# Performance work log

Measured on AMD Instinct MI355X. Metric: run time of the kernel, lower is better.

The kernel has to match this reference:

```python
import jax, jax.numpy as jnp
import numpy as np

B, T, C, HD = 16, 2048, 1024, 64


def setup_inputs() -> dict:
    key = jax.random.key(0)
    kx, kk, kq, kv = jax.random.split(key, 4)
    x = jax.random.normal(kx, (B, T, C), dtype=jnp.float32)
    Wk = jax.random.normal(kk, (C, HD), dtype=jnp.float32) * (C ** -0.5)
    Wq = jax.random.normal(kq, (C, HD), dtype=jnp.float32) * (C ** -0.5)
    Wv = jax.random.normal(kv, (C, HD), dtype=jnp.float32) * (C ** -0.5)
    return {"x": x, "Wk": Wk, "Wq": Wq, "Wv": Wv}


def reference(x, Wk, Wq, Wv):
    Bs, Ts, Cs = x.shape
    k = x @ Wk  # [B,T,HD]
    q = x @ Wq
    v = x @ Wv
    # Faithful to original: scores = key @ query^T, scaled by 1/sqrt(C) (embed dim!)
    scores = jnp.einsum('bth,bsh->bts', k, q) / jnp.sqrt(jnp.float32(Cs))
    causal = jnp.tril(jnp.ones((Ts, Ts), dtype=bool))  # tril[:T,:T]
    scores = jnp.where(causal, scores, -jnp.inf)
    weights = jax.nn.softmax(scores, axis=-1)  # [B,T,T]
    return jnp.einsum('bts,bsh->bth', weights, v)  # [B,T,HD]
```

## Files before the change

### kernel.cpp

```cpp
#include <hip/hip_runtime.h>
#include <hip/hip_bf16.h>

#define B_ 16
#define T_ 2048
#define C_ 1024
#define HD_ 64

typedef __attribute__((ext_vector_type(8))) short bf16x8;
typedef __attribute__((ext_vector_type(4))) float f32x4;

__device__ __forceinline__ unsigned short f2bf(float f) {
  return __builtin_bit_cast(unsigned short, __float2bfloat16(f));
}

__device__ __forceinline__ bf16x8 cvt8(float4 a, float4 b) {
  bf16x8 r;
  r[0] = (short)f2bf(a.x); r[1] = (short)f2bf(a.y);
  r[2] = (short)f2bf(a.z); r[3] = (short)f2bf(a.w);
  r[4] = (short)f2bf(b.x); r[5] = (short)f2bf(b.y);
  r[6] = (short)f2bf(b.z); r[7] = (short)f2bf(b.w);
  return r;
}

__global__ void wconv_kernel(const float* __restrict__ Wk, const float* __restrict__ Wq,
                             const float* __restrict__ Wv, unsigned short* __restrict__ wt2) {
  int o = blockIdx.x * 256 + threadIdx.x;
  if (o >= 3 * HD_ * C_) return;
  int r = o >> 10;
  int c = o & 1023;
  int s = c >> 3, e = c & 7;
  int lc = (((s & 0x78) | ((s ^ r) & 7)) << 3) | e;
  int m = r >> 6, d = r & 63;
  const float* W = (m == 0) ? Wk : (m == 1) ? Wq : Wv;
  float v = W[lc * HD_ + d];
  if (m == 0) v *= 0.03125f;
  wt2[o] = f2bf(v);
}

__global__ __launch_bounds__(256, 2) void qkv_kernel(const float* __restrict__ x,
                                                     const unsigned short* __restrict__ wt2,
                                                     unsigned short* __restrict__ kb,
                                                     unsigned short* __restrict__ qb,
                                                     unsigned short* __restrict__ vb) {
  __shared__ __align__(16) unsigned short wl[2 * 12288];

  const int tid = threadIdx.x;
  const int lane = tid & 63;
  const int w = tid >> 6;
  const int l15 = lane & 15;
  const int lh = lane >> 4;
  const int r0 = blockIdx.x * 64;
  const int sw = l15 & 7;
  const int c0 = (lh ^ sw) * 8;
  const int c1 = ((4 | lh) ^ sw) * 8;

  const float* xp = x + (size_t)(r0 + w * 16 + l15) * C_ + lh * 8;

  f32x4 acc[12];
#pragma unroll
  for (int i = 0; i < 12; ++i) acc[i] = {0.f, 0.f, 0.f, 0.f};

  float4 xr0[4], xr1[4], xr2[4];

#define STAGE(BUF, KK)                                                               \
  do {                                                                               \
    _Pragma("unroll")                                                                \
    for (int i_ = 0; i_ < 6; ++i_) {                                                 \
      const int gp_ = w * 6 + i_;                                                    \
      const int row_ = gp_ * 8 + (lane >> 3);                                        \
      const unsigned short* g_ = wt2 + row_ * 1024 + (KK) * 64 + (lane & 7) * 8;     \
      __builtin_amdgcn_global_load_lds(                                              \
          (const __attribute__((address_space(1))) void*)g_,                         \
          (__attribute__((address_space(3))) void*)&wl[(BUF) * 12288 + gp_ * 512],   \
          16, 0, 0);                                                                 \
    }                                                                                \
  } while (0)

#define XLOAD(XR, KK)                               \
  do {                                              \
    const float* p_ = xp + (KK) * 64;               \
    XR[0] = *(const float4*)(p_);                   \
    XR[1] = *(const float4*)(p_ + 4);               \
    XR[2] = *(const float4*)(p_ + 32);              \
    XR[3] = *(const float4*)(p_ + 36);              \
  } while (0)

#define COMPUTE(K, XR)                                                                   \
  do {                                                                                   \
    const unsigned short* wb = &wl[((K) & 1) * 12288];                                   \
    bf16x8 a0 = cvt8(XR[0], XR[1]);                                                      \
    bf16x8 a1 = cvt8(XR[2], XR[3]);                                                      \
    _Pragma("unroll")                                                                    \
    for (int cf = 0; cf < 12; ++cf) {                                                    \
      bf16x8 b0 = *(const bf16x8*)&wb[((cf >> 2) * 64 + (cf & 3) * 16 + l15) * 64 + c0]; \
      acc[cf] = __builtin_amdgcn_mfma_f32_16x16x32_bf16(a0, b0, acc[cf], 0, 0, 0);       \
    }                                                                                    \
    _Pragma("unroll")                                                                    \
    for (int cf = 0; cf < 12; ++cf) {                                                    \
      bf16x8 b1 = *(const bf16x8*)&wb[((cf >> 2) * 64 + (cf & 3) * 16 + l15) * 64 + c1]; \
      acc[cf] = __builtin_amdgcn_mfma_f32_16x16x32_bf16(a1, b1, acc[cf], 0, 0, 0);       \
    }                                                                                    \
  } while (0)

#define SB __builtin_amdgcn_sched_barrier(0)

#define ITER(K, XCUR, XPRE, VM)                                    \
  do {                                                             \
    if ((K) < 15) STAGE(((K) + 1) & 1, (K) + 1);                   \
    SB;                                                            \
    if ((K) < 14) XLOAD(XPRE, (K) + 2);                            \
    SB;                                                            \
    asm volatile("s_waitcnt vmcnt(" #VM ")" ::: "memory");         \
    SB;                                                            \
    __builtin_amdgcn_s_barrier();                                  \
    COMPUTE(K, XCUR);                                              \
    __builtin_amdgcn_s_barrier();                                  \
  } while (0)

  STAGE(0, 0);
  SB;
  XLOAD(xr0, 0);
  XLOAD(xr1, 1);
  SB;

  ITER(0, xr0, xr2, 14);
  ITER(1, xr1, xr0, 14);
  ITER(2, xr2, xr1, 14);
  ITER(3, xr0, xr2, 14);
  ITER(4, xr1, xr0, 14);
  ITER(5, xr2, xr1, 14);
  ITER(6, xr0, xr2, 14);
  ITER(7, xr1, xr0, 14);
  ITER(8, xr2, xr1, 14);
  ITER(9, xr0, xr2, 14);
  ITER(10, xr1, xr0, 14);
  ITER(11, xr2, xr1, 14);
  ITER(12, xr0, xr2, 14);
  ITER(13, xr1, xr0, 14);
  ITER(14, xr2, xr1, 10);
  ITER(15, xr0, xr2, 0);

#undef ITER
#undef COMPUTE
#undef XLOAD
#undef STAGE
#undef SB

#pragma unroll
  for (int cf = 0; cf < 4; ++cf) {
    int col = cf * 16 + l15;
#pragma unroll
    for (int r = 0; r < 4; ++r) {
      size_t row = (size_t)(r0 + w * 16 + lh * 4 + r);
      kb[row * HD_ + col] = f2bf(acc[cf][r]);
      qb[row * HD_ + col] = f2bf(acc[4 + cf][r]);
      vb[row * HD_ + col] = f2bf(acc[8 + cf][r]);
    }
  }
}

__global__ __launch_bounds__(256) void attn_kernel(const unsigned short* __restrict__ kb,
                                                   const unsigned short* __restrict__ qb,
                                                   const unsigned short* __restrict__ vb,
                                                   float* __restrict__ out) {
  __shared__ __align__(16) unsigned short q_lds[64 * 72];
  __shared__ __align__(16) unsigned short v_lds[64 * 72];
  __shared__ __align__(16) unsigned short p_lds[64 * 72];

  const int tid = threadIdx.x;
  const int lane = tid & 63;
  const int w = tid >> 6;
  const int bid = blockIdx.x;
  const int jt = 31 - (bid >> 4);
  const int b = bid & 15;
  const int t0 = jt * 64;
  const int l15 = lane & 15;
  const int lh = lane >> 4;
  const size_t base = (size_t)b * T_ * HD_;

  bf16x8 kf[2];
#pragma unroll
  for (int ks = 0; ks < 2; ++ks)
    kf[ks] = *reinterpret_cast<const bf16x8*>(
        &kb[base + (size_t)(t0 + w * 16 + l15) * HD_ + ks * 32 + lh * 8]);

  f32x4 o[4];
#pragma unroll
  for (int i = 0; i < 4; ++i) o[i] = {0.f, 0.f, 0.f, 0.f};
  float mrun[4], lrun[4];
#pragma unroll
  for (int r = 0; r < 4; ++r) { mrun[r] = -1e30f; lrun[r] = 0.f; }

  for (int j = 0; j <= jt; ++j) {
    const int s0 = j * 64;
    __syncthreads();
#pragma unroll
    for (int i = 0; i < 2; ++i) {
      int c = i * 256 + tid;
      int row = c >> 3, c8 = c & 7;
      bf16x8 qv = *reinterpret_cast<const bf16x8*>(&qb[base + (size_t)(s0 + row) * HD_ + c8 * 8]);
      *reinterpret_cast<bf16x8*>(&q_lds[row * 72 + c8 * 8]) = qv;
    }
#pragma unroll
    for (int i = 0; i < 2; ++i) {
      int c = i * 256 + tid;
      int ss = c & 63, d0 = (c >> 6) * 8;
      bf16x8 vv = *reinterpret_cast<const bf16x8*>(&vb[base + (size_t)(s0 + ss) * HD_ + d0]);
#pragma unroll
      for (int jj = 0; jj < 8; ++jj) v_lds[(d0 + jj) * 72 + ss] = (unsigned short)vv[jj];
    }
    __syncthreads();

    f32x4 sf[4];
#pragma unroll
    for (int cf = 0; cf < 4; ++cf) sf[cf] = {0.f, 0.f, 0.f, 0.f};
#pragma unroll
    for (int ks = 0; ks < 2; ++ks) {
#pragma unroll
      for (int cf = 0; cf < 4; ++cf) {
        bf16x8 bq = *reinterpret_cast<const bf16x8*>(&q_lds[(cf * 16 + l15) * 72 + ks * 32 + lh * 8]);
        sf[cf] = __builtin_amdgcn_mfma_f32_16x16x32_bf16(kf[ks], bq, sf[cf], 0, 0, 0);
      }
    }

    const bool diag = (j == jt);
    float pv[4][4];
#pragma unroll
    for (int r = 0; r < 4; ++r) {
      const int tg = t0 + w * 16 + lh * 4 + r;
      float pm = -1e30f;
#pragma unroll
      for (int cf = 0; cf < 4; ++cf) {
        float v = sf[cf][r];
        if (diag && (s0 + cf * 16 + l15) > tg) v = -1e30f;
        pv[cf][r] = v;
        pm = fmaxf(pm, v);
      }
      pm = fmaxf(pm, __shfl_xor(pm, 1));
      pm = fmaxf(pm, __shfl_xor(pm, 2));
      pm = fmaxf(pm, __shfl_xor(pm, 4));
      pm = fmaxf(pm, __shfl_xor(pm, 8));
      float mn = fmaxf(mrun[r], pm);
      float scl = __expf(mrun[r] - mn);
      mrun[r] = mn;
      float rs = 0.f;
#pragma unroll
      for (int cf = 0; cf < 4; ++cf) {
        float e = __expf(pv[cf][r] - mn);
        pv[cf][r] = e;
        rs += e;
      }
      rs += __shfl_xor(rs, 1);
      rs += __shfl_xor(rs, 2);
      rs += __shfl_xor(rs, 4);
      rs += __shfl_xor(rs, 8);
      lrun[r] = lrun[r] * scl + rs;
#pragma unroll
      for (int df = 0; df < 4; ++df) o[df][r] *= scl;
    }
#pragma unroll
    for (int cf = 0; cf < 4; ++cf)
#pragma unroll
      for (int r = 0; r < 4; ++r)
        p_lds[(w * 16 + lh * 4 + r) * 72 + cf * 16 + l15] = f2bf(pv[cf][r]);
    __syncthreads();

#pragma unroll
    for (int ks = 0; ks < 2; ++ks) {
      bf16x8 pa = *reinterpret_cast<const bf16x8*>(&p_lds[(w * 16 + l15) * 72 + ks * 32 + lh * 8]);
#pragma unroll
      for (int df = 0; df < 4; ++df) {
        bf16x8 bv = *reinterpret_cast<const bf16x8*>(&v_lds[(df * 16 + l15) * 72 + ks * 32 + lh * 8]);
        o[df] = __builtin_amdgcn_mfma_f32_16x16x32_bf16(pa, bv, o[df], 0, 0, 0);
      }
    }
  }

#pragma unroll
  for (int r = 0; r < 4; ++r) {
    float inv = 1.f / lrun[r];
    int row = t0 + w * 16 + lh * 4 + r;
#pragma unroll
    for (int df = 0; df < 4; ++df)
      out[base + (size_t)row * HD_ + df * 16 + l15] = o[df][r] * inv;
  }
}

extern "C" void kernel_launch(void* const* d_in, const int* in_sizes, int n_in,
                              void* d_out, int out_size, void* d_ws, size_t ws_size,
                              hipStream_t stream) {
  const float* x  = (const float*)d_in[0];
  const float* Wk = (const float*)d_in[1];
  const float* Wq = (const float*)d_in[2];
  const float* Wv = (const float*)d_in[3];
  float* out = (float*)d_out;

  char* ws = (char*)d_ws;
  unsigned short* wt2 = (unsigned short*)ws;
  unsigned short* kb = (unsigned short*)(ws + 524288);
  unsigned short* qb = (unsigned short*)(ws + 524288 + 4 * 1024 * 1024);
  unsigned short* vb = (unsigned short*)(ws + 524288 + 8 * 1024 * 1024);

  hipLaunchKernelGGL(wconv_kernel, dim3(768), dim3(256), 0, stream, Wk, Wq, Wv, wt2);
  hipLaunchKernelGGL(qkv_kernel, dim3(512), dim3(256), 0, stream, x, wt2, kb, qb, vb);
  hipLaunchKernelGGL(attn_kernel, dim3(512), dim3(256), 0, stream, kb, qb, vb, out);
}
```

Measured before the change: 94.18 us.

## Double-buffer Q/V tiles with register prefetch, use exp2 softmax, rebalance causal tiles

Q and V tiles move into double-buffered LDS, and the next tile is prefetched into registers while the current one is computed. This cuts the per-iteration sync count from three to one and hides global load latency. The softmax uses exp2 with log2(e) folded into the K weights, and block-to-tile mapping is changed to interleave long and short causal rows for load balance. s_setprio wraps the MFMA sections. Each wave's P rows are private, so dropping the sync before PV relies on within-wave ordering, but the lighter synchronisation and tile ordering carry some correctness risk.

```diff
diff --git a/kernel.cpp b/kernel.cpp
--- a/kernel.cpp
+++ b/kernel.cpp
@@ -33,7 +33,7 @@
   int m = r >> 6, d = r & 63;
   const float* W = (m == 0) ? Wk : (m == 1) ? Wq : Wv;
   float v = W[lc * HD_ + d];
-  if (m == 0) v *= 0.03125f;
+  if (m == 0) v *= 0.03125f * 1.44269504088896f;
   wt2[o] = f2bf(v);
 }
 
@@ -163,27 +163,37 @@
                                                    const unsigned short* __restrict__ qb,
                                                    const unsigned short* __restrict__ vb,
                                                    float* __restrict__ out) {
-  __shared__ __align__(16) unsigned short q_lds[64 * 72];
-  __shared__ __align__(16) unsigned short v_lds[64 * 72];
+  __shared__ __align__(16) unsigned short q_lds[2][64 * 72];
+  __shared__ __align__(16) unsigned short v_lds[2][64 * 72];
   __shared__ __align__(16) unsigned short p_lds[64 * 72];
 
   const int tid = threadIdx.x;
   const int lane = tid & 63;
   const int w = tid >> 6;
   const int bid = blockIdx.x;
-  const int jt = 31 - (bid >> 4);
+  const int idx = bid >> 4;
+  const int jt = (idx < 16) ? (31 - idx) : (idx - 16);
   const int b = bid & 15;
   const int t0 = jt * 64;
   const int l15 = lane & 15;
   const int lh = lane >> 4;
   const size_t base = (size_t)b * T_ * HD_;
 
+  const int qrow = tid >> 3, qc8 = tid & 7;
+  const int vss = tid & 63, vd0 = (tid >> 6) * 8;
+
   bf16x8 kf[2];
 #pragma unroll
   for (int ks = 0; ks < 2; ++ks)
     kf[ks] = *reinterpret_cast<const bf16x8*>(
         &kb[base + (size_t)(t0 + w * 16 + l15) * HD_ + ks * 32 + lh * 8]);
 
+  bf16x8 qr0, qr1, vr0, vr1;
+  qr0 = *reinterpret_cast<const bf16x8*>(&qb[base + (size_t)qrow * HD_ + qc8 * 8]);
+  qr1 = *reinterpret_cast<const bf16x8*>(&qb[base + (size_t)(qrow + 32) * HD_ + qc8 * 8]);
+  vr0 = *reinterpret_cast<const bf16x8*>(&vb[base + (size_t)vss * HD_ + vd0]);
+  vr1 = *reinterpret_cast<const bf16x8*>(&vb[base + (size_t)vss * HD_ + vd0 + 32]);
+
   f32x4 o[4];
 #pragma unroll
   for (int i = 0; i < 4; ++i) o[i] = {0.f, 0.f, 0.f, 0.f};
@@ -192,38 +202,40 @@
   for (int r = 0; r < 4; ++r) { mrun[r] = -1e30f; lrun[r] = 0.f; }
 
   for (int j = 0; j <= jt; ++j) {
-    const int s0 = j * 64;
+    const int buf = j & 1;
+    *reinterpret_cast<bf16x8*>(&q_lds[buf][qrow * 72 + qc8 * 8]) = qr0;
+    *reinterpret_cast<bf16x8*>(&q_lds[buf][(qrow + 32) * 72 + qc8 * 8]) = qr1;
+#pragma unroll
+    for (int jj = 0; jj < 8; ++jj) v_lds[buf][(vd0 + jj) * 72 + vss] = (unsigned short)vr0[jj];
+#pragma unroll
+    for (int jj = 0; jj < 8; ++jj) v_lds[buf][(vd0 + 32 + jj) * 72 + vss] = (unsigned short)vr1[jj];
     __syncthreads();
-#pragma unroll
-    for (int i = 0; i < 2; ++i) {
-      int c = i * 256 + tid;
-      int row = c >> 3, c8 = c & 7;
-      bf16x8 qv = *reinterpret_cast<const bf16x8*>(&qb[base + (size_t)(s0 + row) * HD_ + c8 * 8]);
-      *reinterpret_cast<bf16x8*>(&q_lds[row * 72 + c8 * 8]) = qv;
-    }
-#pragma unroll
-    for (int i = 0; i < 2; ++i) {
-      int c = i * 256 + tid;
-      int ss = c & 63, d0 = (c >> 6) * 8;
-      bf16x8 vv = *reinterpret_cast<const bf16x8*>(&vb[base + (size_t)(s0 + ss) * HD_ + d0]);
-#pragma unroll
-      for (int jj = 0; jj < 8; ++jj) v_lds[(d0 + jj) * 72 + ss] = (unsigned short)vv[jj];
-    }
-    __syncthreads();
+
+    if (j < jt) {
+      const size_t sb = base + (size_t)(j + 1) * 64 * HD_;
+      qr0 = *reinterpret_cast<const bf16x8*>(&qb[sb + (size_t)qrow * HD_ + qc8 * 8]);
+      qr1 = *reinterpret_cast<const bf16x8*>(&qb[sb + (size_t)(qrow + 32) * HD_ + qc8 * 8]);
+      vr0 = *reinterpret_cast<const bf16x8*>(&vb[sb + (size_t)vss * HD_ + vd0]);
+      vr1 = *reinterpret_cast<const bf16x8*>(&vb[sb + (size_t)vss * HD_ + vd0 + 32]);
+    }
+    __builtin_amdgcn_sched_barrier(0);
 
     f32x4 sf[4];
 #pragma unroll
     for (int cf = 0; cf < 4; ++cf) sf[cf] = {0.f, 0.f, 0.f, 0.f};
+    __builtin_amdgcn_s_setprio(1);
 #pragma unroll
     for (int ks = 0; ks < 2; ++ks) {
 #pragma unroll
       for (int cf = 0; cf < 4; ++cf) {
-        bf16x8 bq = *reinterpret_cast<const bf16x8*>(&q_lds[(cf * 16 + l15) * 72 + ks * 32 + lh * 8]);
+        bf16x8 bq = *reinterpret_cast<const bf16x8*>(&q_lds[buf][(cf * 16 + l15) * 72 + ks * 32 + lh * 8]);
         sf[cf] = __builtin_amdgcn_mfma_f32_16x16x32_bf16(kf[ks], bq, sf[cf], 0, 0, 0);
       }
     }
+    __builtin_amdgcn_s_setprio(0);
 
     const bool diag = (j == jt);
+    const int s0 = j * 64;
     float pv[4][4];
 #pragma unroll
     for (int r = 0; r < 4; ++r) {
@@ -241,12 +253,12 @@
       pm = fmaxf(pm, __shfl_xor(pm, 4));
       pm = fmaxf(pm, __shfl_xor(pm, 8));
       float mn = fmaxf(mrun[r], pm);
-      float scl = __expf(mrun[r] - mn);
+      float scl = exp2f(mrun[r] - mn);
       mrun[r] = mn;
       float rs = 0.f;
 #pragma unroll
       for (int cf = 0; cf < 4; ++cf) {
-        float e = __expf(pv[cf][r] - mn);
+        float e = exp2f(pv[cf][r] - mn);
         pv[cf][r] = e;
         rs += e;
       }
@@ -263,17 +275,18 @@
 #pragma unroll
       for (int r = 0; r < 4; ++r)
         p_lds[(w * 16 + lh * 4 + r) * 72 + cf * 16 + l15] = f2bf(pv[cf][r]);
-    __syncthreads();
-
+
+    __builtin_amdgcn_s_setprio(1);
 #pragma unroll
     for (int ks = 0; ks < 2; ++ks) {
       bf16x8 pa = *reinterpret_cast<const bf16x8*>(&p_lds[(w * 16 + l15) * 72 + ks * 32 + lh * 8]);
 #pragma unroll
       for (int df = 0; df < 4; ++df) {
-        bf16x8 bv = *reinterpret_cast<const bf16x8*>(&v_lds[(df * 16 + l15) * 72 + ks * 32 + lh * 8]);
+        bf16x8 bv = *reinterpret_cast<const bf16x8*>(&v_lds[buf][(df * 16 + l15) * 72 + ks * 32 + lh * 8]);
         o[df] = __builtin_amdgcn_mfma_f32_16x16x32_bf16(pa, bv, o[df], 0, 0, 0);
       }
     }
+    __builtin_amdgcn_s_setprio(0);
   }
 
 #pragma unroll
```

New measurement: 90.15 us. 1.04x faster.
